# Performance work log

Hardware: AMD Instinct MI355X
Metric: run time of the kernel (lower is better)

The kernel has to match this reference:

```python
import jax, jax.numpy as jnp
import numpy as np

N_VER = 163842
IN_FEATS = 64
OUT_FEATS = 64


def setup_inputs() -> dict:
    key = jax.random.key(0)
    k1, k2, k3, k4 = jax.random.split(key, 4)
    x = jax.random.normal(k1, (N_VER, IN_FEATS), dtype=jnp.float32)
    hex_in = jax.random.randint(k2, (N_VER * 7,), 0, N_VER, dtype=jnp.int64)
    # Linear(7*in_feats, out_feats): weight stored as [7*in_feats, out_feats]
    W = jax.random.normal(k3, (7 * IN_FEATS, OUT_FEATS), dtype=jnp.float32) * (1.0 / np.sqrt(7 * IN_FEATS))
    b = jax.random.normal(k4, (OUT_FEATS,), dtype=jnp.float32) * 0.01
    return {"x": x, "hex_in": hex_in, "W": W, "b": b}


def reference(x, hex_in, W, b):
    n_ver = x.shape[0]
    # Gather 7-ring neighbor features: [7*n_ver, in_feats] -> [n_ver, 7*in_feats]
    x_new = x[hex_in].reshape(n_ver, 7 * x.shape[1])
    # Dense linear layer
    return x_new @ W + b
```

## Files before the change

### kernel.cpp

```cpp
#include <hip/hip_runtime.h>

#define N_VERT 163842
#define N8_X   1310736
#define NBLK   512
#define ROWS_PER_BLK 320

typedef float  f32x4  __attribute__((ext_vector_type(4)));
typedef short  s16x8  __attribute__((ext_vector_type(8)));

__device__ __forceinline__ unsigned short f2bf(float f) {
  union { float f; unsigned int u; } c; c.f = f;
  unsigned int u = c.u;
  u += 0x7FFFu + ((u >> 16) & 1u);
  return (unsigned short)(u >> 16);
}

__device__ __forceinline__ s16x8 cvt8(const f32x4 a, const f32x4 b) {
  s16x8 h;
  h[0] = (short)f2bf(a[0]); h[1] = (short)f2bf(a[1]);
  h[2] = (short)f2bf(a[2]); h[3] = (short)f2bf(a[3]);
  h[4] = (short)f2bf(b[0]); h[5] = (short)f2bf(b[1]);
  h[6] = (short)f2bf(b[2]); h[7] = (short)f2bf(b[3]);
  return h;
}

__global__ void detect64(const unsigned int* __restrict__ hexw, int* __restrict__ flag) {
  __shared__ int any;
  if (threadIdx.x == 0) any = 0;
  __syncthreads();
  if (hexw[2 * threadIdx.x + 1] != 0u) any = 1;
  __syncthreads();
  if (threadIdx.x == 0) *flag = (any == 0) ? 1 : 0;
}

__global__ __launch_bounds__(256) void prep(
    const float* __restrict__ x, const unsigned int* __restrict__ hexw,
    const float* __restrict__ W,
    unsigned short* __restrict__ Wf, unsigned short* __restrict__ xbf,
    int* __restrict__ flag)
{
  const int b = blockIdx.x, tid = threadIdx.x;

  if (b == 0) {
    __shared__ int any;
    if (tid == 0) any = 0;
    __syncthreads();
    if (hexw[2 * tid + 1] != 0u) any = 1;
    __syncthreads();
    if (tid == 0) *flag = (any == 0) ? 1 : 0;
  }
  if (b >= 1 && b <= 112) {
    const int t   = (b - 1) * 256 + tid;
    const int e   = t & 7;
    const int col = (t >> 3) & 63;
    const int hi  = (t >> 9) & 3;
    const int ks  = t >> 11;
    Wf[t] = f2bf(W[(ks * 32 + hi * 8 + e) * 64 + col]);
  }
  const int stride = gridDim.x * 256;
  for (int i = b * 256 + tid; i < N8_X; i += stride) {
    const f32x4* s = (const f32x4*)(x + (size_t)i * 8);
    *(s16x8*)(xbf + (size_t)i * 8) = cvt8(s[0], s[1]);
  }
}

template <int BF>
__global__ __launch_bounds__(256) void hexconv7(
    const void* __restrict__ xsrc,
    const unsigned int* __restrict__ hexw,
    const void* __restrict__ wsrc,
    const float* __restrict__ bias,
    float* __restrict__ out,
    const int* __restrict__ flag)
{
  __shared__ unsigned short Wl[28672];

  const int tid = threadIdx.x;
  const int wv  = tid >> 6;
  const int ln  = tid & 63;
  const int lo  = ln & 15;
  const int hi  = ln >> 4;
  const int is64 = flag ? *flag : 1;

  if (BF) {
    const s16x8* wsv = (const s16x8*)wsrc;
#pragma unroll
    for (int it = 0; it < 14; ++it)
      ((s16x8*)Wl)[it * 256 + tid] = wsv[it * 256 + tid];
  } else {
    const float* W = (const float*)wsrc;
    for (int it = 0; it < 112; ++it) {
      const int t   = it * 256 + tid;
      const int e   = t & 7;
      const int col = (t >> 3) & 63;
      const int hif = (t >> 9) & 3;
      const int ks  = t >> 11;
      Wl[t] = f2bf(W[(ks * 32 + hif * 8 + e) * 64 + col]);
    }
  }
  __syncthreads();

  const char* xbase = (const char*)xsrc;
  const char* hexb  = (const char*)hexw;
  const char* Wb    = (const char*)Wl + (hi * 64 + lo) * 16;

  float bval[4];
#pragma unroll
  for (int nt = 0; nt < 4; ++nt) bval[nt] = bias[nt * 16 + lo];

  const int B0 = blockIdx.x * ROWS_PER_BLK;
  const int base3 = (wv < 2) ? wv * 96 : 192 + (wv - 2) * 64;
  const int rb0 = B0 + base3;
  const int rb1 = rb0 + 32;
  const bool special = (blockIdx.x == NBLK - 1) && (wv == 2);
  const bool three = (wv < 2) || special;
  const int rb2 = special ? 163840 : rb0 + 64;

  const int shf = 2 + is64;
  const int obs = BF ? 7 : 8;

#define LOAD_OFF(O0, O1, rb_)                                                  \
  do {                                                                         \
    int ra = (rb_) + lo;        ra = (ra < N_VERT) ? ra : (N_VERT - 1);        \
    int rbx = (rb_) + 16 + lo;  rbx = (rbx < N_VERT) ? rbx : (N_VERT - 1);     \
    const char* ipa = hexb + ((size_t)((unsigned)ra * 7u) << shf);             \
    const char* ipb = hexb + ((size_t)((unsigned)rbx * 7u) << shf);            \
    _Pragma("unroll")                                                          \
    for (int j = 0; j < 7; ++j) {                                              \
      (O0)[j] = (*(const unsigned int*)(ipa + ((size_t)j << shf))) << obs;     \
      (O1)[j] = (*(const unsigned int*)(ipb + ((size_t)j << shf))) << obs;     \
    }                                                                          \
  } while (0)

#define LOAD_S(S, O0, O1, jj)                                                  \
  do {                                                                         \
    const char* p0 = xbase + (size_t)(O0)[jj];                                 \
    const char* p1 = xbase + (size_t)(O1)[jj];                                 \
    if (BF) {                                                                  \
      S##00 = *(const s16x8*)(p0 + hi * 16);                                   \
      S##01 = *(const s16x8*)(p0 + 64 + hi * 16);                              \
      S##10 = *(const s16x8*)(p1 + hi * 16);                                   \
      S##11 = *(const s16x8*)(p1 + 64 + hi * 16);                              \
    } else {                                                                   \
      const f32x4* q0 = (const f32x4*)(p0 + hi * 32);                          \
      const f32x4* q1 = (const f32x4*)(p1 + hi * 32);                          \
      S##00 = cvt8(q0[0], q0[1]);                                              \
      S##01 = cvt8(*(const f32x4*)(p0 + 128 + hi * 32),                        \
                   *(const f32x4*)(p0 + 144 + hi * 32));                       \
      S##10 = cvt8(q1[0], q1[1]);                                              \
      S##11 = cvt8(*(const f32x4*)(p1 + 128 + hi * 32),                        \
                   *(const f32x4*)(p1 + 144 + hi * 32));                       \
    }                                                                          \
  } while (0)

#define MFMA_J(jj, S)                                                          \
  do {                                                                         \
    _Pragma("unroll")                                                          \
    for (int nt = 0; nt < 4; ++nt) {                                           \
      const s16x8 bf0 = *(const s16x8*)(Wb + (2 * (jj)) * 4096 + nt * 256);    \
      acc0[nt] = __builtin_amdgcn_mfma_f32_16x16x32_bf16(S##00, bf0, acc0[nt], 0, 0, 0); \
      acc1[nt] = __builtin_amdgcn_mfma_f32_16x16x32_bf16(S##10, bf0, acc1[nt], 0, 0, 0); \
    }                                                                          \
    _Pragma("unroll")                                                          \
    for (int nt = 0; nt < 4; ++nt) {                                           \
      const s16x8 bf1 = *(const s16x8*)(Wb + (2 * (jj) + 1) * 4096 + nt * 256);\
      acc0[nt] = __builtin_amdgcn_mfma_f32_16x16x32_bf16(S##01, bf1, acc0[nt], 0, 0, 0); \
      acc1[nt] = __builtin_amdgcn_mfma_f32_16x16x32_bf16(S##11, bf1, acc1[nt], 0, 0, 0); \
    }                                                                          \
  } while (0)

#define STORES(RB)                                                             \
  do {                                                                         \
    _Pragma("unroll")                                                          \
    for (int i = 0; i < 4; ++i) {                                              \
      const int row0 = (RB) + hi * 4 + i;                                      \
      if (row0 < N_VERT) {                                                     \
        float* orow = out + (size_t)row0 * 64;                                 \
        _Pragma("unroll")                                                      \
        for (int nt = 0; nt < 4; ++nt) orow[nt * 16 + lo] = acc0[nt][i] + bval[nt]; \
      }                                                                        \
      const int row1 = (RB) + 16 + hi * 4 + i;                                 \
      if (row1 < N_VERT) {                                                     \
        float* orow = out + (size_t)row1 * 64;                                 \
        _Pragma("unroll")                                                      \
        for (int nt = 0; nt < 4; ++nt) orow[nt * 16 + lo] = acc1[nt][i] + bval[nt]; \
      }                                                                        \
    }                                                                          \
  } while (0)

#define CHUNK(RB, ENT, ALT, OC0, OC1, DO_NOFF, ON0, ON1, RBN, DO_NA)           \
  do {                                                                         \
    _Pragma("unroll")                                                          \
    for (int nt = 0; nt < 4; ++nt) { acc0[nt] = (f32x4){0,0,0,0}; acc1[nt] = (f32x4){0,0,0,0}; } \
    LOAD_S(ALT, OC0, OC1, 1);                                                  \
    if (DO_NOFF) LOAD_OFF(ON0, ON1, RBN);                                      \
    MFMA_J(0, ENT);  LOAD_S(ENT, OC0, OC1, 2);                                 \
    MFMA_J(1, ALT);  LOAD_S(ALT, OC0, OC1, 3);                                 \
    MFMA_J(2, ENT);  LOAD_S(ENT, OC0, OC1, 4);                                 \
    MFMA_J(3, ALT);  LOAD_S(ALT, OC0, OC1, 5);                                 \
    MFMA_J(4, ENT);  LOAD_S(ENT, OC0, OC1, 6);                                 \
    MFMA_J(5, ALT);                                                            \
    if (DO_NA) LOAD_S(ALT, ON0, ON1, 0);                                       \
    MFMA_J(6, ENT);                                                            \
    STORES(RB);                                                                \
  } while (0)

  unsigned int offA0[7], offA1[7], offB0[7], offB1[7];
  s16x8 sA00, sA01, sA10, sA11, sB00, sB01, sB10, sB11;
  f32x4 acc0[4], acc1[4];

  LOAD_OFF(offA0, offA1, rb0);
  LOAD_S(sA, offA0, offA1, 0);

  CHUNK(rb0, sA, sB, offA0, offA1, true, offB0, offB1, rb1, true);
  CHUNK(rb1, sB, sA, offB0, offB1, three, offA0, offA1, rb2, three);
  if (three)
    CHUNK(rb2, sA, sB, offA0, offA1, false, offB0, offB1, rb2, false);

#undef LOAD_OFF
#undef LOAD_S
#undef MFMA_J
#undef STORES
#undef CHUNK
}

extern "C" void kernel_launch(void* const* d_in, const int* in_sizes, int n_in,
                              void* d_out, int out_size, void* d_ws, size_t ws_size,
                              hipStream_t stream) {
  const float*        x    = (const float*)d_in[0];
  const unsigned int* hexw = (const unsigned int*)d_in[1];
  const float*        W    = (const float*)d_in[2];
  const float*        b    = (const float*)d_in[3];
  float*              out  = (float*)d_out;

  const size_t WS_NEED = 65536 + (size_t)N_VERT * 64 * 2;

  if (ws_size >= WS_NEED) {
    int*            flag = (int*)d_ws;
    unsigned short* Wf   = (unsigned short*)((char*)d_ws + 4096);
    unsigned short* xbf  = (unsigned short*)((char*)d_ws + 65536);
    prep<<<2048, 256, 0, stream>>>(x, hexw, W, Wf, xbf, flag);
    hexconv7<1><<<NBLK, 256, 0, stream>>>(xbf, hexw, Wf, b, out, flag);
  } else {
    int* flag = (ws_size >= 4) ? (int*)d_ws : nullptr;
    if (flag) detect64<<<1, 256, 0, stream>>>(hexw, flag);
    hexconv7<0><<<NBLK, 256, 0, stream>>>(x, hexw, W, b, out, flag);
  }
}
```

Measured before the change: 45.50 us.

## Transpose neighbor indices in prep and gather rows coalesced through LDS bounce

The prep kernel now also writes a transposed, pre-shifted copy of the neighbor index table, so the main kernel reads indices for 32 vertices of one ring position as a contiguous block and stages them in LDS. A new hexconv8 kernel gathers each bf16 feature row with eight lanes reading 16 bytes each, so one row is a contiguous 128-byte access. It writes the rows into a swizzled per-wave LDS bounce buffer and reads the MFMA operands back from it. This replaces the old scattered per-lane row reads, at the price of an extra pass over the index array in prep, more LDS traffic, and explicit waitcnt fences.

Measured after the change: 45.57 us. Within noise of the previous version (+0.2%).

```diff
diff --git a/kernel.cpp b/kernel.cpp
--- a/kernel.cpp
+++ b/kernel.cpp
@@ -36,19 +36,19 @@
 __global__ __launch_bounds__(256) void prep(
     const float* __restrict__ x, const unsigned int* __restrict__ hexw,
     const float* __restrict__ W,
-    unsigned short* __restrict__ Wf, unsigned short* __restrict__ xbf,
-    int* __restrict__ flag)
+    unsigned short* __restrict__ Wf, unsigned int* __restrict__ hexT,
+    unsigned short* __restrict__ xbf, int* __restrict__ flag)
 {
   const int b = blockIdx.x, tid = threadIdx.x;
 
-  if (b == 0) {
-    __shared__ int any;
-    if (tid == 0) any = 0;
-    __syncthreads();
-    if (hexw[2 * tid + 1] != 0u) any = 1;
-    __syncthreads();
-    if (tid == 0) *flag = (any == 0) ? 1 : 0;
-  }
+  __shared__ int anyb;
+  if (tid == 0) anyb = 0;
+  __syncthreads();
+  if (hexw[2 * tid + 1] != 0u) anyb = 1;
+  __syncthreads();
+  const int is64 = (anyb == 0) ? 1 : 0;
+  if (b == 0 && tid == 0) *flag = is64;
+
   if (b >= 1 && b <= 112) {
     const int t   = (b - 1) * 256 + tid;
     const int e   = t & 7;
@@ -57,7 +57,17 @@
     const int ks  = t >> 11;
     Wf[t] = f2bf(W[(ks * 32 + hi * 8 + e) * 64 + col]);
   }
+
   const int stride = gridDim.x * 256;
+
+  const int T7 = 7 * N_VERT;
+  for (int t = b * 256 + tid; t < T7; t += stride) {
+    const int j = t / N_VERT;
+    const int v = t - j * N_VERT;
+    const unsigned int idx = hexw[(unsigned int)(v * 7 + j) << is64];
+    hexT[t] = idx << 7;
+  }
+
   for (int i = b * 256 + tid; i < N8_X; i += stride) {
     const f32x4* s = (const f32x4*)(x + (size_t)i * 8);
     *(s16x8*)(xbf + (size_t)i * 8) = cvt8(s[0], s[1]);
@@ -66,15 +76,11 @@
 
 template <int BF>
 __global__ __launch_bounds__(256) void hexconv7(
-    const void* __restrict__ xsrc,
-    const unsigned int* __restrict__ hexw,
-    const void* __restrict__ wsrc,
-    const float* __restrict__ bias,
-    float* __restrict__ out,
-    const int* __restrict__ flag)
+    const void* __restrict__ xsrc, const unsigned int* __restrict__ hexw,
+    const void* __restrict__ wsrc, const float* __restrict__ bias,
+    float* __restrict__ out, const int* __restrict__ flag)
 {
   __shared__ unsigned short Wl[28672];
-
   const int tid = threadIdx.x;
   const int wv  = tid >> 6;
   const int ln  = tid & 63;
@@ -82,12 +88,7 @@
   const int hi  = ln >> 4;
   const int is64 = flag ? *flag : 1;
 
-  if (BF) {
-    const s16x8* wsv = (const s16x8*)wsrc;
-#pragma unroll
-    for (int it = 0; it < 14; ++it)
-      ((s16x8*)Wl)[it * 256 + tid] = wsv[it * 256 + tid];
-  } else {
+  {
     const float* W = (const float*)wsrc;
     for (int it = 0; it < 112; ++it) {
       const int t   = it * 256 + tid;
@@ -115,57 +116,161 @@
   const bool special = (blockIdx.x == NBLK - 1) && (wv == 2);
   const bool three = (wv < 2) || special;
   const int rb2 = special ? 163840 : rb0 + 64;
-
   const int shf = 2 + is64;
-  const int obs = BF ? 7 : 8;
-
-#define LOAD_OFF(O0, O1, rb_)                                                  \
-  do {                                                                         \
-    int ra = (rb_) + lo;        ra = (ra < N_VERT) ? ra : (N_VERT - 1);        \
-    int rbx = (rb_) + 16 + lo;  rbx = (rbx < N_VERT) ? rbx : (N_VERT - 1);     \
-    const char* ipa = hexb + ((size_t)((unsigned)ra * 7u) << shf);             \
-    const char* ipb = hexb + ((size_t)((unsigned)rbx * 7u) << shf);            \
-    _Pragma("unroll")                                                          \
-    for (int j = 0; j < 7; ++j) {                                              \
-      (O0)[j] = (*(const unsigned int*)(ipa + ((size_t)j << shf))) << obs;     \
-      (O1)[j] = (*(const unsigned int*)(ipb + ((size_t)j << shf))) << obs;     \
+
+  f32x4 acc0[4], acc1[4];
+  for (int cc = 0; cc < 3; ++cc) {
+    if (cc == 2 && !three) break;
+    const int rb = (cc == 0) ? rb0 : (cc == 1) ? rb1 : rb2;
+#pragma unroll
+    for (int nt = 0; nt < 4; ++nt) { acc0[nt] = (f32x4){0,0,0,0}; acc1[nt] = (f32x4){0,0,0,0}; }
+    int ra = rb + lo;        ra = (ra < N_VERT) ? ra : (N_VERT - 1);
+    int rbx = rb + 16 + lo;  rbx = (rbx < N_VERT) ? rbx : (N_VERT - 1);
+    const char* ipa = hexb + ((size_t)((unsigned)ra * 7u) << shf);
+    const char* ipb = hexb + ((size_t)((unsigned)rbx * 7u) << shf);
+#pragma unroll
+    for (int j = 0; j < 7; ++j) {
+      const size_t o0 = (size_t)(*(const unsigned int*)(ipa + ((size_t)j << shf))) << 8;
+      const size_t o1 = (size_t)(*(const unsigned int*)(ipb + ((size_t)j << shf))) << 8;
+      const char* p0 = xbase + o0;
+      const char* p1 = xbase + o1;
+      const f32x4* q0 = (const f32x4*)(p0 + hi * 32);
+      const f32x4* q1 = (const f32x4*)(p1 + hi * 32);
+      const s16x8 a00 = cvt8(q0[0], q0[1]);
+      const s16x8 a01 = cvt8(*(const f32x4*)(p0 + 128 + hi * 32), *(const f32x4*)(p0 + 144 + hi * 32));
+      const s16x8 a10 = cvt8(q1[0], q1[1]);
+      const s16x8 a11 = cvt8(*(const f32x4*)(p1 + 128 + hi * 32), *(const f32x4*)(p1 + 144 + hi * 32));
+#pragma unroll
+      for (int nt = 0; nt < 4; ++nt) {
+        const s16x8 bf0 = *(const s16x8*)(Wb + (2 * j) * 4096 + nt * 256);
+        acc0[nt] = __builtin_amdgcn_mfma_f32_16x16x32_bf16(a00, bf0, acc0[nt], 0, 0, 0);
+        acc1[nt] = __builtin_amdgcn_mfma_f32_16x16x32_bf16(a10, bf0, acc1[nt], 0, 0, 0);
+      }
+#pragma unroll
+      for (int nt = 0; nt < 4; ++nt) {
+        const s16x8 bf1 = *(const s16x8*)(Wb + (2 * j + 1) * 4096 + nt * 256);
+        acc0[nt] = __builtin_amdgcn_mfma_f32_16x16x32_bf16(a01, bf1, acc0[nt], 0, 0, 0);
+        acc1[nt] = __builtin_amdgcn_mfma_f32_16x16x32_bf16(a11, bf1, acc1[nt], 0, 0, 0);
+      }
+    }
+#pragma unroll
+    for (int i = 0; i < 4; ++i) {
+      const int row0 = rb + hi * 4 + i;
+      if (row0 < N_VERT) {
+        float* orow = out + (size_t)row0 * 64;
+#pragma unroll
+        for (int nt = 0; nt < 4; ++nt) orow[nt * 16 + lo] = acc0[nt][i] + bval[nt];
+      }
+      const int row1 = rb + 16 + hi * 4 + i;
+      if (row1 < N_VERT) {
+        float* orow = out + (size_t)row1 * 64;
+#pragma unroll
+        for (int nt = 0; nt < 4; ++nt) orow[nt * 16 + lo] = acc1[nt][i] + bval[nt];
+      }
+    }
+  }
+}
+
+__global__ __launch_bounds__(256) void hexconv8(
+    const unsigned short* __restrict__ xbf,
+    const unsigned int* __restrict__ hexT,
+    const unsigned short* __restrict__ Wf,
+    const float* __restrict__ bias,
+    float* __restrict__ out)
+{
+  __shared__ unsigned short Wl[28672];
+  __shared__ unsigned int   offsb[4][2][224];
+  __shared__ unsigned short bounce[4][2048];
+
+  const int tid = threadIdx.x;
+  const int wv  = tid >> 6;
+  const int ln  = tid & 63;
+  const int lo  = ln & 15;
+  const int hi  = ln >> 4;
+  const int oct = ln >> 3;
+  const int qr16 = (ln & 7) * 16;
+
+  {
+    const s16x8* wsv = (const s16x8*)Wf;
+#pragma unroll
+    for (int it = 0; it < 14; ++it)
+      ((s16x8*)Wl)[it * 256 + tid] = wsv[it * 256 + tid];
+  }
+  __syncthreads();
+
+  const char* xbase = (const char*)xbf;
+  const char* Wb    = (const char*)Wl + (hi * 64 + lo) * 16;
+  char*       bnc   = (char*)&bounce[wv][0];
+  char*       bncw  = bnc + oct * 128 + (qr16 ^ (oct << 4));
+  const int   rswz  = (lo & 7) << 4;
+  const int   fb0   = lo * 128 + ((hi * 16) ^ rswz);
+  const int   fb1   = lo * 128 + ((64 + hi * 16) ^ rswz);
+
+  float bval[4];
+#pragma unroll
+  for (int nt = 0; nt < 4; ++nt) bval[nt] = bias[nt * 16 + lo];
+
+  const int B0 = blockIdx.x * ROWS_PER_BLK;
+  const int base3 = (wv < 2) ? wv * 96 : 192 + (wv - 2) * 64;
+  const int rb0 = B0 + base3;
+  const int rb1 = rb0 + 32;
+  const bool special = (blockIdx.x == NBLK - 1) && (wv == 2);
+  const bool three = (wv < 2) || special;
+  const int rb2 = special ? 163840 : rb0 + 64;
+
+#define STAGE_OFFS(P, V0N)                                                     \
+  do {                                                                         \
+    _Pragma("unroll")                                                          \
+    for (int it_ = 0; it_ < 4; ++it_) {                                        \
+      const int t_ = it_ * 64 + ln;                                            \
+      if (t_ < 224) {                                                          \
+        const int jj_ = t_ >> 5;                                               \
+        int v_ = (V0N) + (t_ & 31);                                            \
+        v_ = (v_ < N_VERT) ? v_ : (N_VERT - 1);                                \
+        offsb[wv][P][t_] = hexT[jj_ * N_VERT + v_];                            \
+      }                                                                        \
     }                                                                          \
   } while (0)
 
-#define LOAD_S(S, O0, O1, jj)                                                  \
-  do {                                                                         \
-    const char* p0 = xbase + (size_t)(O0)[jj];                                 \
-    const char* p1 = xbase + (size_t)(O1)[jj];                                 \
-    if (BF) {                                                                  \
-      S##00 = *(const s16x8*)(p0 + hi * 16);                                   \
-      S##01 = *(const s16x8*)(p0 + 64 + hi * 16);                              \
-      S##10 = *(const s16x8*)(p1 + hi * 16);                                   \
-      S##11 = *(const s16x8*)(p1 + 64 + hi * 16);                              \
-    } else {                                                                   \
-      const f32x4* q0 = (const f32x4*)(p0 + hi * 32);                          \
-      const f32x4* q1 = (const f32x4*)(p1 + hi * 32);                          \
-      S##00 = cvt8(q0[0], q0[1]);                                              \
-      S##01 = cvt8(*(const f32x4*)(p0 + 128 + hi * 32),                        \
-                   *(const f32x4*)(p0 + 144 + hi * 32));                       \
-      S##10 = cvt8(q1[0], q1[1]);                                              \
-      S##11 = cvt8(*(const f32x4*)(p1 + 128 + hi * 32),                        \
-                   *(const f32x4*)(p1 + 144 + hi * 32));                       \
-    }                                                                          \
-  } while (0)
-
-#define MFMA_J(jj, S)                                                          \
-  do {                                                                         \
+#define GATH(GS, P, JJ)                                                        \
+  do {                                                                         \
+    const unsigned int o0_ = offsb[wv][P][(JJ) * 32 + oct];                    \
+    const unsigned int o1_ = offsb[wv][P][(JJ) * 32 + 8 + oct];                \
+    const unsigned int o2_ = offsb[wv][P][(JJ) * 32 + 16 + oct];               \
+    const unsigned int o3_ = offsb[wv][P][(JJ) * 32 + 24 + oct];               \
+    GS##0 = *(const s16x8*)(xbase + o0_ + qr16);                               \
+    GS##1 = *(const s16x8*)(xbase + o1_ + qr16);                               \
+    GS##2 = *(const s16x8*)(xbase + o2_ + qr16);                               \
+    GS##3 = *(const s16x8*)(xbase + o3_ + qr16);                               \
+  } while (0)
+
+#define DSW(GS)                                                                \
+  do {                                                                         \
+    *(s16x8*)(bncw)        = GS##0;                                            \
+    *(s16x8*)(bncw + 1024) = GS##1;                                            \
+    *(s16x8*)(bncw + 2048) = GS##2;                                            \
+    *(s16x8*)(bncw + 3072) = GS##3;                                            \
+  } while (0)
+
+#define FENCE asm volatile("s_waitcnt lgkmcnt(0)" ::: "memory")
+
+#define MFMA_J(jj)                                                             \
+  do {                                                                         \
+    const s16x8 S00 = *(const s16x8*)(bnc + fb0);                              \
+    const s16x8 S01 = *(const s16x8*)(bnc + fb1);                              \
+    const s16x8 S10 = *(const s16x8*)(bnc + 2048 + fb0);                       \
+    const s16x8 S11 = *(const s16x8*)(bnc + 2048 + fb1);                       \
     _Pragma("unroll")                                                          \
     for (int nt = 0; nt < 4; ++nt) {                                           \
       const s16x8 bf0 = *(const s16x8*)(Wb + (2 * (jj)) * 4096 + nt * 256);    \
-      acc0[nt] = __builtin_amdgcn_mfma_f32_16x16x32_bf16(S##00, bf0, acc0[nt], 0, 0, 0); \
-      acc1[nt] = __builtin_amdgcn_mfma_f32_16x16x32_bf16(S##10, bf0, acc1[nt], 0, 0, 0); \
+      acc0[nt] = __builtin_amdgcn_mfma_f32_16x16x32_bf16(S00, bf0, acc0[nt], 0, 0, 0); \
+      acc1[nt] = __builtin_amdgcn_mfma_f32_16x16x32_bf16(S10, bf0, acc1[nt], 0, 0, 0); \
     }                                                                          \
     _Pragma("unroll")                                                          \
     for (int nt = 0; nt < 4; ++nt) {                                           \
       const s16x8 bf1 = *(const s16x8*)(Wb + (2 * (jj) + 1) * 4096 + nt * 256);\
-      acc0[nt] = __builtin_amdgcn_mfma_f32_16x16x32_bf16(S##01, bf1, acc0[nt], 0, 0, 0); \
-      acc1[nt] = __builtin_amdgcn_mfma_f32_16x16x32_bf16(S##11, bf1, acc1[nt], 0, 0, 0); \
+      acc0[nt] = __builtin_amdgcn_mfma_f32_16x16x32_bf16(S01, bf1, acc0[nt], 0, 0, 0); \
+      acc1[nt] = __builtin_amdgcn_mfma_f32_16x16x32_bf16(S11, bf1, acc1[nt], 0, 0, 0); \
     }                                                                          \
   } while (0)
 
@@ -188,37 +293,45 @@
     }                                                                          \
   } while (0)
 
-#define CHUNK(RB, ENT, ALT, OC0, OC1, DO_NOFF, ON0, ON1, RBN, DO_NA)           \
-  do {                                                                         \
+#define CHUNK(V0, P, GE, GO, HASN, V0N)                                        \
+  do {                                                                         \
+    if (HASN) STAGE_OFFS((P) ^ 1, V0N);                                        \
     _Pragma("unroll")                                                          \
     for (int nt = 0; nt < 4; ++nt) { acc0[nt] = (f32x4){0,0,0,0}; acc1[nt] = (f32x4){0,0,0,0}; } \
-    LOAD_S(ALT, OC0, OC1, 1);                                                  \
-    if (DO_NOFF) LOAD_OFF(ON0, ON1, RBN);                                      \
-    MFMA_J(0, ENT);  LOAD_S(ENT, OC0, OC1, 2);                                 \
-    MFMA_J(1, ALT);  LOAD_S(ALT, OC0, OC1, 3);                                 \
-    MFMA_J(2, ENT);  LOAD_S(ENT, OC0, OC1, 4);                                 \
-    MFMA_J(3, ALT);  LOAD_S(ALT, OC0, OC1, 5);                                 \
-    MFMA_J(4, ENT);  LOAD_S(ENT, OC0, OC1, 6);                                 \
-    MFMA_J(5, ALT);                                                            \
-    if (DO_NA) LOAD_S(ALT, ON0, ON1, 0);                                       \
-    MFMA_J(6, ENT);                                                            \
-    STORES(RB);                                                                \
-  } while (0)
-
-  unsigned int offA0[7], offA1[7], offB0[7], offB1[7];
-  s16x8 sA00, sA01, sA10, sA11, sB00, sB01, sB10, sB11;
+    GATH(GO, P, 2);                                                            \
+    MFMA_J(0); FENCE; DSW(GE);                                                 \
+    GATH(GE, P, 3);                                                            \
+    MFMA_J(1); FENCE; DSW(GO);                                                 \
+    GATH(GO, P, 4);                                                            \
+    MFMA_J(2); FENCE; DSW(GE);                                                 \
+    GATH(GE, P, 5);                                                            \
+    MFMA_J(3); FENCE; DSW(GO);                                                 \
+    GATH(GO, P, 6);                                                            \
+    MFMA_J(4); FENCE; DSW(GE);                                                 \
+    if (HASN) GATH(GE, (P) ^ 1, 0);                                            \
+    MFMA_J(5); FENCE; DSW(GO);                                                 \
+    if (HASN) GATH(GO, (P) ^ 1, 1);                                            \
+    MFMA_J(6);                                                                 \
+    STORES(V0);                                                                \
+    if (HASN) { FENCE; DSW(GE); }                                              \
+  } while (0)
+
+  s16x8 gA0, gA1, gA2, gA3, gB0, gB1, gB2, gB3;
   f32x4 acc0[4], acc1[4];
 
-  LOAD_OFF(offA0, offA1, rb0);
-  LOAD_S(sA, offA0, offA1, 0);
-
-  CHUNK(rb0, sA, sB, offA0, offA1, true, offB0, offB1, rb1, true);
-  CHUNK(rb1, sB, sA, offB0, offB1, three, offA0, offA1, rb2, three);
-  if (three)
-    CHUNK(rb2, sA, sB, offA0, offA1, false, offB0, offB1, rb2, false);
-
-#undef LOAD_OFF
-#undef LOAD_S
+  STAGE_OFFS(0, rb0);
+  GATH(gA, 0, 0);
+  DSW(gA);
+  GATH(gB, 0, 1);
+
+  CHUNK(rb0, 0, gB, gA, true, rb1);
+  CHUNK(rb1, 1, gA, gB, three, rb2);
+  if (three) CHUNK(rb2, 0, gB, gA, false, rb2);
+
+#undef STAGE_OFFS
+#undef GATH
+#undef DSW
+#undef FENCE
 #undef MFMA_J
 #undef STORES
 #undef CHUNK
@@ -233,14 +346,18 @@
   const float*        b    = (const float*)d_in[3];
   float*              out  = (float*)d_out;
 
-  const size_t WS_NEED = 65536 + (size_t)N_VERT * 64 * 2;
+  const size_t OFF_WF   = 4096;
+  const size_t OFF_HEXT = 65536;
+  const size_t OFF_XBF  = 4653568;
+  const size_t WS_NEED  = OFF_XBF + (size_t)N_VERT * 64 * 2;
 
   if (ws_size >= WS_NEED) {
     int*            flag = (int*)d_ws;
-    unsigned short* Wf   = (unsigned short*)((char*)d_ws + 4096);
-    unsigned short* xbf  = (unsigned short*)((char*)d_ws + 65536);
-    prep<<<2048, 256, 0, stream>>>(x, hexw, W, Wf, xbf, flag);
-    hexconv7<1><<<NBLK, 256, 0, stream>>>(xbf, hexw, Wf, b, out, flag);
+    unsigned short* Wf   = (unsigned short*)((char*)d_ws + OFF_WF);
+    unsigned int*   hexT = (unsigned int*)((char*)d_ws + OFF_HEXT);
+    unsigned short* xbf  = (unsigned short*)((char*)d_ws + OFF_XBF);
+    prep<<<2048, 256, 0, stream>>>(x, hexw, W, Wf, hexT, xbf, flag);
+    hexconv8<<<NBLK, 256, 0, stream>>>(xbf, hexT, Wf, b, out);
   } else {
     int* flag = (ws_size >= 4) ? (int*)d_ws : nullptr;
     if (flag) detect64<<<1, 256, 0, stream>>>(hexw, flag);
```
